# Optimization experiments

Measured on AMD Instinct MI355X. Metric: run time of the kernel, lower is better.

## Reference

```python
import jax, jax.numpy as jnp
import numpy as np

EPS_CR = 0.5      # eps in coding rate
ETA = 0.5
LAMBDA_LAP = 0.3
LN_EPS = 1e-5


def setup_inputs() -> dict:
    key = jax.random.key(0)
    ks = jax.random.split(key, 8)
    n, in_dim, out_dim, d_sub, K1 = 8192, 256, 128, 64, 3
    H = jax.random.normal(ks[0], (n, in_dim), jnp.float32)
    hop_feats = jax.random.normal(ks[1], (K1, n, in_dim), jnp.float32)
    L = jax.random.normal(ks[2], (n, n), jnp.float32) * 0.01
    W_stack = jax.random.normal(ks[3], (K1, d_sub, in_dim), jnp.float32) * 0.05
    W_out = jax.random.normal(ks[4], (out_dim, in_dim), jnp.float32) * 0.05
    threshold = jnp.full((out_dim,), 0.05, jnp.float32)
    ln_gamma = jnp.ones((out_dim,), jnp.float32)
    ln_beta = jnp.zeros((out_dim,), jnp.float32)
    tau = jnp.asarray(1.0, jnp.float32)
    return {"H": H, "hop_feats": hop_feats, "L": L, "W_stack": W_stack,
            "W_out": W_out, "threshold": threshold, "ln_gamma": ln_gamma,
            "ln_beta": ln_beta, "tau": tau}


def reference(H, hop_feats, L, W_stack, W_out, threshold, ln_gamma, ln_beta, tau):
    n = H.shape[0]
    d = W_stack.shape[1]
    coeff = d / (n * EPS_CR * EPS_CR)
    # per-hop subspace projections: Z [K+1, n, d]
    Z = jnp.einsum('knf,kdf->knd', hop_feats, W_stack)
    # shared Gram M = I + coeff * Z^T Z  [K+1, d, d]
    G = jnp.einsum('knd,kne->kde', Z, Z)
    M = jnp.eye(d, dtype=Z.dtype)[None] + coeff * G
    # coding rates via batched slogdet
    _, logdet = jnp.linalg.slogdet(M)
    R = 0.5 * logdet                                    # [K+1]
    # delta_R: first entry is R[0], rest are successive diffs
    delta_R = R - jnp.concatenate([jnp.zeros((1,), R.dtype), R[:-1]])
    dR_norm = (delta_R - delta_R.mean()) / (jnp.std(delta_R, ddof=1) + 1e-6)
    w = jax.nn.softmax(dR_norm / tau)                   # [K+1]
    # coding-rate gradients: g_Z = coeff * Z @ M^{-1} via batched solve
    g_Z = coeff * jnp.linalg.solve(M, jnp.swapaxes(Z, 1, 2))  # [K+1, d, n]
    # g_H[k] = g_Z[k]^T @ W[k]; weighted sum over hops -> [n, in_dim]
    grad_contrib = jnp.einsum('k,kdn,kdf->nf', w, g_Z, W_stack)
    H_half = H + ETA * grad_contrib - ETA * LAMBDA_LAP * (L @ H)
    # in_dim != out_dim -> project
    H_pre = H_half @ W_out.T                            # [n, out_dim]
    thr = jnp.abs(threshold)[None, :]
    H_soft = jnp.sign(H_pre) * jnp.maximum(jnp.abs(H_pre) - thr, 0.0)
    # LayerNorm over last dim
    mu = H_soft.mean(-1, keepdims=True)
    var = jnp.mean((H_soft - mu) ** 2, -1, keepdims=True)
    H_out = (H_soft - mu) * jax.lax.rsqrt(var + LN_EPS) * ln_gamma + ln_beta
    return (H_out, w, jax.lax.stop_gradient(dR_norm), jax.lax.stop_gradient(delta_R))
```

## Files before the change

kernel.cpp:

```cpp
#include <hip/hip_runtime.h>
#include <hip/hip_bf16.h>
#include <math.h>


#define COEFF 0.03125f
#define SCL_LAP (-0.15f)

typedef __attribute__((ext_vector_type(8))) short short8;
typedef __attribute__((ext_vector_type(4))) float f32x4;

__device__ __forceinline__ unsigned short f2bf_bits(float f) {
  unsigned int u = __float_as_uint(f);
  unsigned int r = (u + 0x7fffu + ((u >> 16) & 1u)) >> 16;
  return (unsigned short)r;
}

__global__ __launch_bounds__(256) void gemm_tile(
    const float* __restrict__ A, const float* __restrict__ B,
    float* __restrict__ C, const float* __restrict__ addC,
    const float* __restrict__ scale_ptr,
    int K, int lda, int ldb, int ldc, int ldadd,
    long sA, long sB, long sC, int transB) {
  __shared__ __align__(16) float As[16][68];
  __shared__ __align__(16) float Bs[16][68];
  const int tid = threadIdx.x;
  const int tx = tid & 15, ty = tid >> 4;
  const int m0 = blockIdx.y * 64, n0 = blockIdx.x * 64;
  const int b = blockIdx.z;
  A += (size_t)b * sA; B += (size_t)b * sB; C += (size_t)b * sC;
  float cc[4][4];
#pragma unroll
  for (int i = 0; i < 4; ++i)
#pragma unroll
    for (int j = 0; j < 4; ++j) cc[i][j] = 0.f;
  const int lr = tid >> 2, lc = (tid & 3) << 2;
  for (int k0 = 0; k0 < K; k0 += 16) {
    float4 av = *(const float4*)(A + (size_t)(m0 + lr) * lda + k0 + lc);
    As[lc][lr] = av.x; As[lc + 1][lr] = av.y; As[lc + 2][lr] = av.z; As[lc + 3][lr] = av.w;
    if (transB) {
      float4 bv = *(const float4*)(B + (size_t)(n0 + lr) * ldb + k0 + lc);
      Bs[lc][lr] = bv.x; Bs[lc + 1][lr] = bv.y; Bs[lc + 2][lr] = bv.z; Bs[lc + 3][lr] = bv.w;
    } else {
      int kk = tid & 15, n4 = (tid >> 4) << 2;
      float4 bv = *(const float4*)(B + (size_t)(k0 + kk) * ldb + n0 + n4);
      *(float4*)&Bs[kk][n4] = bv;
    }
    __syncthreads();
#pragma unroll
    for (int kk = 0; kk < 16; ++kk) {
      float4 a4 = *(const float4*)&As[kk][ty * 4];
      float4 b4 = *(const float4*)&Bs[kk][tx * 4];
      float a[4] = {a4.x, a4.y, a4.z, a4.w};
      float bb[4] = {b4.x, b4.y, b4.z, b4.w};
#pragma unroll
      for (int i = 0; i < 4; ++i)
#pragma unroll
        for (int j = 0; j < 4; ++j) cc[i][j] = fmaf(a[i], bb[j], cc[i][j]);
    }
    __syncthreads();
  }
  float scale = scale_ptr ? scale_ptr[b] : 1.0f;
#pragma unroll
  for (int i = 0; i < 4; ++i)
#pragma unroll
    for (int j = 0; j < 4; ++j) {
      int m = m0 + ty * 4 + i, n = n0 + tx * 4 + j;
      float v = cc[i][j] * scale;
      if (addC) v += addC[(size_t)m * ldadd + n];
      C[(size_t)m * ldc + n] = v;
    }
}

__global__ __launch_bounds__(256) void gram_kernel(const float* __restrict__ Z,
                                                   float* __restrict__ Gpart) {
  __shared__ __align__(16) float Zs[64][68];
  const int k = blockIdx.y, tid = threadIdx.x;
  const int d0 = (tid & 15) * 4, e0 = (tid >> 4) * 4;
  float acc[4][4];
#pragma unroll
  for (int i = 0; i < 4; ++i)
#pragma unroll
    for (int j = 0; j < 4; ++j) acc[i][j] = 0.f;
  for (int c = 0; c < 4; ++c) {
    int nb = blockIdx.x * 256 + c * 64;
    for (int idx = tid; idx < 1024; idx += 256) {
      int rr = idx >> 4, c4 = (idx & 15) * 4;
      float4 v = *(const float4*)(Z + (size_t)(nb + rr) * 192 + k * 64 + c4);
      *(float4*)&Zs[rr][c4] = v;
    }
    __syncthreads();
    for (int rr = 0; rr < 64; ++rr) {
      float4 zd4 = *(const float4*)&Zs[rr][d0];
      float4 ze4 = *(const float4*)&Zs[rr][e0];
      float zd[4] = {zd4.x, zd4.y, zd4.z, zd4.w};
      float ze[4] = {ze4.x, ze4.y, ze4.z, ze4.w};
#pragma unroll
      for (int i = 0; i < 4; ++i)
#pragma unroll
        for (int j = 0; j < 4; ++j) acc[i][j] = fmaf(zd[i], ze[j], acc[i][j]);
    }
    __syncthreads();
  }
  float* g = Gpart + (size_t)(k * 32 + blockIdx.x) * 4096;
#pragma unroll
  for (int i = 0; i < 4; ++i)
#pragma unroll
    for (int j = 0; j < 4; ++j) g[(d0 + i) * 64 + (e0 + j)] = acc[i][j];
}

__device__ __forceinline__ float blocksum256(float v, volatile float* scr) {
#pragma unroll
  for (int o = 32; o; o >>= 1) v += __shfl_xor(v, o);
  __syncthreads();
  if ((threadIdx.x & 63) == 0) scr[threadIdx.x >> 6] = v;
  __syncthreads();
  return scr[0] + scr[1] + scr[2] + scr[3];
}

__device__ __forceinline__ void gemm64s(const float* X, const float* Y,
                                        float acc[4][4]) {
  const int tx = threadIdx.x & 15, ty = threadIdx.x >> 4;
#pragma unroll
  for (int i = 0; i < 4; ++i)
#pragma unroll
    for (int j = 0; j < 4; ++j) acc[i][j] = 0.f;
  for (int kk = 0; kk < 64; ++kk) {
    float4 a4 = *(const float4*)&X[kk * 64 + ty * 4];
    float4 b4 = *(const float4*)&Y[kk * 64 + tx * 4];
    float a[4] = {a4.x, a4.y, a4.z, a4.w};
    float bb[4] = {b4.x, b4.y, b4.z, b4.w};
#pragma unroll
    for (int i = 0; i < 4; ++i)
#pragma unroll
      for (int j = 0; j < 4; ++j) acc[i][j] = fmaf(a[i], bb[j], acc[i][j]);
  }
}

__device__ __forceinline__ void wb64(float* D, const float acc[4][4]) {
  const int tx = threadIdx.x & 15, ty = threadIdx.x >> 4;
#pragma unroll
  for (int i = 0; i < 4; ++i)
#pragma unroll
    for (int j = 0; j < 4; ++j) D[(ty * 4 + i) * 64 + tx * 4 + j] = acc[i][j];
}

__device__ __forceinline__ float dot64(const float* X, const float* Y, float* scr) {
  const int tx = threadIdx.x & 15, ty = threadIdx.x >> 4;
  float v = 0.f;
#pragma unroll
  for (int i = 0; i < 4; ++i)
#pragma unroll
    for (int j = 0; j < 4; ++j) {
      int idx = (ty * 4 + i) * 64 + tx * 4 + j;
      v += X[idx] * Y[idx];
    }
  return blocksum256(v, scr);
}

__global__ __launch_bounds__(256) void fused_big(
    const float* __restrict__ Lp, const unsigned short* __restrict__ HpT,
    float* __restrict__ Pbuf, const float* __restrict__ Gpart,
    float* __restrict__ Minv, float* __restrict__ Rout) {
  __shared__ __align__(16) float smem[12304];
  const int tid = threadIdx.x;

  if (blockIdx.x >= 3) {
    unsigned short (*As)[40] = (unsigned short(*)[40])smem;
    unsigned short (*Bs)[40] = (unsigned short(*)[40])(smem + 2560);
    const int g = blockIdx.x - 3;
    const int m0 = (g & 63) * 128;
    const int split = g >> 6;
    const int kbase = split * 1024;
    const int wave = tid >> 6, lane = tid & 63;
    const int ar = tid >> 1, ah = (tid & 1) * 16;
    const size_t lrow = (size_t)(m0 + ar) * 8192;
    const size_t brow = (size_t)ar * 8192;
    f32x4 acc[2][8];
#pragma unroll
    for (int i = 0; i < 2; ++i)
#pragma unroll
      for (int j = 0; j < 8; ++j) acc[i][j] = (f32x4){0.f, 0.f, 0.f, 0.f};
    float4 apf[4];
    uint4 bpf[2];
    {
      const float* ap = Lp + lrow + kbase + ah;
      apf[0] = *(const float4*)(ap); apf[1] = *(const float4*)(ap + 4);
      apf[2] = *(const float4*)(ap + 8); apf[3] = *(const float4*)(ap + 12);
      const unsigned short* bp = HpT + brow + kbase + ah;
      bpf[0] = *(const uint4*)(bp); bpf[1] = *(const uint4*)(bp + 8);
    }
    const int quad = lane >> 4, mcol = lane & 15;
    for (int step = 0; step < 32; ++step) {
      __syncthreads();
      {
        __attribute__((aligned(16))) unsigned short tmp[16];
        const float* f = (const float*)apf;
#pragma unroll
        for (int i = 0; i < 16; ++i) tmp[i] = f2bf_bits(f[i]);
        *(uint4*)&As[ar][ah] = *(const uint4*)&tmp[0];
        *(uint4*)&As[ar][ah + 8] = *(const uint4*)&tmp[8];
        *(uint4*)&Bs[ar][ah] = bpf[0];
        *(uint4*)&Bs[ar][ah + 8] = bpf[1];
      }
      __syncthreads();
      if (step < 31) {
        int kc = kbase + (step + 1) * 32;
        const float* ap = Lp + lrow + kc + ah;
        apf[0] = *(const float4*)(ap); apf[1] = *(const float4*)(ap + 4);
        apf[2] = *(const float4*)(ap + 8); apf[3] = *(const float4*)(ap + 12);
        const unsigned short* bp = HpT + brow + kc + ah;
        bpf[0] = *(const uint4*)(bp); bpf[1] = *(const uint4*)(bp + 8);
      }
      short8 af0 = *(const short8*)&As[wave * 32 + mcol][quad * 8];
      short8 af1 = *(const short8*)&As[wave * 32 + 16 + mcol][quad * 8];
#pragma unroll
      for (int nt = 0; nt < 8; ++nt) {
        short8 bf = *(const short8*)&Bs[nt * 16 + mcol][quad * 8];
        acc[0][nt] = __builtin_amdgcn_mfma_f32_16x16x32_bf16(af0, bf, acc[0][nt], 0, 0, 0);
        acc[1][nt] = __builtin_amdgcn_mfma_f32_16x16x32_bf16(af1, bf, acc[1][nt], 0, 0, 0);
      }
    }
    float* P = Pbuf + (size_t)split * 1048576;
#pragma unroll
    for (int mt = 0; mt < 2; ++mt)
#pragma unroll
      for (int nt = 0; nt < 8; ++nt)
#pragma unroll
        for (int r = 0; r < 4; ++r) {
          int grow = m0 + wave * 32 + mt * 16 + quad * 4 + r;
          int gcol = nt * 16 + mcol;
          P[(size_t)grow * 128 + gcol] = acc[mt][nt][r];
        }
    return;
  }

  const int k = blockIdx.x;
  float* B0 = smem;
  float* B1 = smem + 4096;
  float* B2 = smem + 8192;
  float* scr = smem + 12288;
  for (int i = tid; i < 4096; i += 256) {
    float s = 0.f;
    const float* gp = Gpart + (size_t)k * 32 * 4096 + i;
    for (int b = 0; b < 32; ++b) s += gp[b * 4096];
    B0[i] = COEFF * s + ((i >> 6) == (i & 63) ? 1.f : 0.f);
  }
  __syncthreads();
  if (tid < 64) {
    float rs = 0.f, dg = B0[tid * 65];
    for (int j = 0; j < 64; ++j) rs += fabsf(B0[j * 64 + tid]);
    float lo = 2.f * dg - rs, hi = rs;
#pragma unroll
    for (int o = 32; o; o >>= 1) {
      lo = fminf(lo, __shfl_xor(lo, o));
      hi = fmaxf(hi, __shfl_xor(hi, o));
    }
    if (tid == 0) scr[4] = 0.5f * (fmaxf(lo, 1.f) + hi);
  }
  __syncthreads();
  const float alpha = scr[4], inva = 1.f / alpha;
  for (int i = tid; i < 4096; i += 256) {
    int r = i >> 6, c = i & 63;
    B0[i] = B0[i] * inva - (r == c ? 1.f : 0.f);
  }
  __syncthreads();
  const int tx = tid & 15, ty = tid >> 4;
  float v1 = 0.f, v2 = 0.f;
#pragma unroll
  for (int i = 0; i < 4; ++i)
#pragma unroll
    for (int j = 0; j < 4; ++j) {
      int r = ty * 4 + i, c = tx * 4 + j;
      float e = B0[r * 64 + c];
      if (r == c) v1 += e;
      v2 += e * e;
    }
  float t1 = blocksum256(v1, scr);
  float t2 = blocksum256(v2, scr);
  float acc[4][4];
  gemm64s(B0, B0, acc); __syncthreads(); wb64(B1, acc); __syncthreads();
  float t3 = dot64(B1, B0, scr);
  float t4 = dot64(B1, B1, scr);
  gemm64s(B1, B0, acc); __syncthreads(); wb64(B2, acc); __syncthreads();
  float t5 = dot64(B2, B1, scr);
  float t6 = dot64(B2, B2, scr);
  gemm64s(B1, B1, acc);
  {
    float v7 = 0.f, v8 = 0.f;
#pragma unroll
    for (int i = 0; i < 4; ++i)
#pragma unroll
      for (int j = 0; j < 4; ++j) {
        int idx = (ty * 4 + i) * 64 + tx * 4 + j;
        v7 += acc[i][j] * B2[idx];
        v8 += acc[i][j] * acc[i][j];
      }
    float t7 = blocksum256(v7, scr);
    float t8 = blocksum256(v8, scr);
    if (tid == 0) {
      float ld = 64.f * logf(alpha) + t1 - t2 * 0.5f + t3 / 3.f - t4 * 0.25f
                 + t5 * 0.2f - t6 / 6.f + t7 / 7.f - t8 * 0.125f;
      Rout[k] = 0.5f * ld;
    }
  }
  for (int i = tid; i < 4096; i += 256) {
    int r = i >> 6, c = i & 63;
    B1[i] = (r == c ? 1.f : 0.f) - B0[i];
  }
  __syncthreads();
  for (int it = 0; it < 2; ++it) {
    gemm64s(B0, B1, acc);
    __syncthreads();
    {
#pragma unroll
      for (int i = 0; i < 4; ++i)
#pragma unroll
        for (int j = 0; j < 4; ++j) {
          int idx = (ty * 4 + i) * 64 + tx * 4 + j;
          B2[idx] = acc[i][j] + B1[idx];
        }
    }
    __syncthreads();
    gemm64s(B1, B2, acc);
    __syncthreads();
    {
#pragma unroll
      for (int i = 0; i < 4; ++i)
#pragma unroll
        for (int j = 0; j < 4; ++j) {
          int idx = (ty * 4 + i) * 64 + tx * 4 + j;
          B1[idx] = 2.f * B1[idx] - acc[i][j];
        }
    }
    __syncthreads();
  }
  for (int i = tid; i < 4096; i += 256) Minv[k * 4096 + i] = B1[i] * inva;
}

__global__ void small_w(const float* __restrict__ R, const float* __restrict__ tauP,
                        float* __restrict__ tail, float* __restrict__ sb) {
  if (threadIdx.x != 0) return;
  float R0 = R[0], R1 = R[1], R2 = R[2];
  float d0 = R0, d1 = R1 - R0, d2 = R2 - R1;
  float mean = (d0 + d1 + d2) * (1.f / 3.f);
  float e0 = d0 - mean, e1 = d1 - mean, e2 = d2 - mean;
  float sd = sqrtf((e0 * e0 + e1 * e1 + e2 * e2) * 0.5f) + 1e-6f;
  float n0 = e0 / sd, n1 = e1 / sd, n2 = e2 / sd;
  float tau = tauP[0];
  float x0 = n0 / tau, x1 = n1 / tau, x2 = n2 / tau;
  float mx = fmaxf(x0, fmaxf(x1, x2));
  float w0 = expf(x0 - mx), w1 = expf(x1 - mx), w2 = expf(x2 - mx);
  float s = w0 + w1 + w2;
  w0 /= s; w1 /= s; w2 /= s;
  tail[0] = w0; tail[1] = w1; tail[2] = w2;
  tail[3] = n0; tail[4] = n1; tail[5] = n2;
  tail[6] = d0; tail[7] = d1; tail[8] = d2;
  sb[0] = 0.015625f * w0; sb[1] = 0.015625f * w1; sb[2] = 0.015625f * w2;
}

__global__ __launch_bounds__(256) void transpose_cvt(const float* __restrict__ Hp,
                                                     unsigned short* __restrict__ HpT) {
  __shared__ float T[32][33];
  const int cb = blockIdx.x, rb = blockIdx.y, tid = threadIdx.x;
  int r = tid >> 3, c4 = (tid & 7) * 4;
  float4 v = *(const float4*)(Hp + (size_t)(rb * 32 + r) * 128 + cb * 32 + c4);
  T[r][c4] = v.x; T[r][c4 + 1] = v.y; T[r][c4 + 2] = v.z; T[r][c4 + 3] = v.w;
  __syncthreads();
  int c = tid >> 3, r4 = (tid & 7) * 4;
  ushort4 u;
  u.x = f2bf_bits(T[r4][c]); u.y = f2bf_bits(T[r4 + 1][c]);
  u.z = f2bf_bits(T[r4 + 2][c]); u.w = f2bf_bits(T[r4 + 3][c]);
  *(ushort4*)(HpT + (size_t)(cb * 32 + c) * 8192 + rb * 32 + r4) = u;
}

__global__ __launch_bounds__(256) void finish_kernel(
    const float* __restrict__ pre, const float* __restrict__ Pbuf,
    const float* __restrict__ thr, const float* __restrict__ gamma,
    const float* __restrict__ beta, float* __restrict__ out) {
  const int lane = threadIdx.x & 63;
  const int row = blockIdx.x * 4 + (threadIdx.x >> 6);
  const size_t off = (size_t)row * 128;
  float l0 = 0.f, l1 = 0.f;
#pragma unroll
  for (int s = 0; s < 8; ++s) {
    l0 += Pbuf[s * 1048576 + off + lane];
    l1 += Pbuf[s * 1048576 + off + lane + 64];
  }
  float x0 = pre[off + lane] + SCL_LAP * l0;
  float x1 = pre[off + lane + 64] + SCL_LAP * l1;
  float t0 = fabsf(thr[lane]), t1 = fabsf(thr[lane + 64]);
  float a0 = fmaxf(fabsf(x0) - t0, 0.f); float s0 = (x0 >= 0.f) ? a0 : -a0;
  float a1 = fmaxf(fabsf(x1) - t1, 0.f); float s1 = (x1 >= 0.f) ? a1 : -a1;
  float sum = s0 + s1;
#pragma unroll
  for (int o = 32; o; o >>= 1) sum += __shfl_xor(sum, o);
  float mean = sum * (1.f / 128.f);
  float d0 = s0 - mean, d1 = s1 - mean;
  float ss = d0 * d0 + d1 * d1;
#pragma unroll
  for (int o = 32; o; o >>= 1) ss += __shfl_xor(ss, o);
  float inv = rsqrtf(ss * (1.f / 128.f) + 1e-5f);
  out[off + lane] = d0 * inv * gamma[lane] + beta[lane];
  out[off + lane + 64] = d1 * inv * gamma[lane + 64] + beta[lane + 64];
}

extern "C" void kernel_launch(void* const* d_in, const int* in_sizes, int n_in,
                              void* d_out, int out_size, void* d_ws, size_t ws_size,
                              hipStream_t stream) {
  const float* H = (const float*)d_in[0];
  const float* hop = (const float*)d_in[1];
  const float* L = (const float*)d_in[2];
  const float* Wst = (const float*)d_in[3];
  const float* Wout = (const float*)d_in[4];
  const float* thr = (const float*)d_in[5];
  const float* gamma = (const float*)d_in[6];
  const float* beta = (const float*)d_in[7];
  const float* tau = (const float*)d_in[8];
  float* out = (float*)d_out;

  float* ws = (float*)d_ws;
  float* Zbuf = ws;
  float* Hp = Zbuf + 1572864;
  float* pre = Hp + 1048576;
  float* Gpart = pre + 1048576;
  float* Minv = Gpart + 393216;
  float* Rb = Minv + 12288;
  float* sb = Rb + 16;
  float* Pb = sb + 16;
  float* QT = Pb + 24576;
  float* Pbuf = QT + 24576;
  unsigned short* HpT = (unsigned short*)(Pbuf + 8388608);

  gemm_tile<<<dim3(2, 128, 1), 256, 0, stream>>>(
      H, Wout, Hp, nullptr, nullptr, 256, 256, 256, 128, 0, 0L, 0L, 0L, 1);
  transpose_cvt<<<dim3(4, 256), 256, 0, stream>>>(Hp, HpT);
  gemm_tile<<<dim3(1, 128, 3), 256, 0, stream>>>(
      hop, Wst, Zbuf, nullptr, nullptr, 256, 256, 256, 192, 0,
      2097152L, 16384L, 64L, 1);
  gram_kernel<<<dim3(32, 3), 256, 0, stream>>>(Zbuf, Gpart);
  gemm_tile<<<dim3(1, 2, 3), 256, 0, stream>>>(
      Wout, Wst, Pb, nullptr, nullptr, 256, 256, 256, 64, 0,
      0L, 16384L, 8192L, 1);
  fused_big<<<dim3(515), 256, 0, stream>>>(L, HpT, Pbuf, Gpart, Minv, Rb);
  small_w<<<dim3(1), 64, 0, stream>>>(Rb, tau, out + 1048576, sb);
  gemm_tile<<<dim3(1, 2, 3), 256, 0, stream>>>(
      Pb, Minv, QT, nullptr, sb, 64, 64, 64, 192, 0,
      8192L, 4096L, 64L, 0);
  gemm_tile<<<dim3(2, 128, 1), 256, 0, stream>>>(
      Zbuf, QT, pre, Hp, nullptr, 192, 192, 192, 128, 128, 0L, 0L, 0L, 1);
  finish_kernel<<<dim3(2048), 256, 0, stream>>>(pre, Pbuf, thr, gamma, beta, out);

  (void)in_sizes; (void)n_in; (void)out_size; (void)ws_size;
}
```

Measured before the change: 559.8 us.

## Fuse projection/transpose, Z/Gram, final GEMM/LayerNorm and double-buffer L GEMM

Fuses the H@Wout projection with the bf16 transpose, the per-hop Z projection with the Gram partial sums, and the final Z@QT GEMM with the Laplacian reduction, soft-threshold and LayerNorm. The fused_big bf16 MFMA loop now uses two LDS buffers with a two-step prefetch, so there is one barrier per step instead of two. Together these drop three launches and the round trips of Hp, Z and the pre buffer through global memory. In exchange the Gram partials grow to 128 per hop, making the reduction in fused_big longer, and the L GEMM needs more LDS and registers.

```diff
diff --git a/kernel.cpp b/kernel.cpp
--- a/kernel.cpp
+++ b/kernel.cpp
@@ -17,9 +17,8 @@
 
 __global__ __launch_bounds__(256) void gemm_tile(
     const float* __restrict__ A, const float* __restrict__ B,
-    float* __restrict__ C, const float* __restrict__ addC,
-    const float* __restrict__ scale_ptr,
-    int K, int lda, int ldb, int ldc, int ldadd,
+    float* __restrict__ C, const float* __restrict__ scale_ptr,
+    int K, int lda, int ldb, int ldc,
     long sA, long sB, long sC, int transB) {
   __shared__ __align__(16) float As[16][68];
   __shared__ __align__(16) float Bs[16][68];
@@ -63,49 +62,120 @@
 #pragma unroll
   for (int i = 0; i < 4; ++i)
 #pragma unroll
-    for (int j = 0; j < 4; ++j) {
-      int m = m0 + ty * 4 + i, n = n0 + tx * 4 + j;
-      float v = cc[i][j] * scale;
-      if (addC) v += addC[(size_t)m * ldadd + n];
-      C[(size_t)m * ldc + n] = v;
-    }
-}
-
-__global__ __launch_bounds__(256) void gram_kernel(const float* __restrict__ Z,
-                                                   float* __restrict__ Gpart) {
-  __shared__ __align__(16) float Zs[64][68];
-  const int k = blockIdx.y, tid = threadIdx.x;
+    for (int j = 0; j < 4; ++j)
+      C[(size_t)(m0 + ty * 4 + i) * ldc + n0 + tx * 4 + j] = cc[i][j] * scale;
+}
+
+__global__ __launch_bounds__(256) void hp_kernel(
+    const float* __restrict__ H, const float* __restrict__ Wout,
+    float* __restrict__ Hp, unsigned short* __restrict__ HpT) {
+  __shared__ __align__(16) float As[16][68];
+  __shared__ __align__(16) float Bs[16][68];
+  const int tid = threadIdx.x;
+  const int tx = tid & 15, ty = tid >> 4;
+  const int m0 = blockIdx.y * 64, n0 = blockIdx.x * 64;
+  float cc[4][4];
+#pragma unroll
+  for (int i = 0; i < 4; ++i)
+#pragma unroll
+    for (int j = 0; j < 4; ++j) cc[i][j] = 0.f;
+  const int lr = tid >> 2, lc = (tid & 3) << 2;
+  for (int k0 = 0; k0 < 256; k0 += 16) {
+    float4 av = *(const float4*)(H + (size_t)(m0 + lr) * 256 + k0 + lc);
+    As[lc][lr] = av.x; As[lc + 1][lr] = av.y; As[lc + 2][lr] = av.z; As[lc + 3][lr] = av.w;
+    float4 bv = *(const float4*)(Wout + (size_t)(n0 + lr) * 256 + k0 + lc);
+    Bs[lc][lr] = bv.x; Bs[lc + 1][lr] = bv.y; Bs[lc + 2][lr] = bv.z; Bs[lc + 3][lr] = bv.w;
+    __syncthreads();
+#pragma unroll
+    for (int kk = 0; kk < 16; ++kk) {
+      float4 a4 = *(const float4*)&As[kk][ty * 4];
+      float4 b4 = *(const float4*)&Bs[kk][tx * 4];
+      float a[4] = {a4.x, a4.y, a4.z, a4.w};
+      float bb[4] = {b4.x, b4.y, b4.z, b4.w};
+#pragma unroll
+      for (int i = 0; i < 4; ++i)
+#pragma unroll
+        for (int j = 0; j < 4; ++j) cc[i][j] = fmaf(a[i], bb[j], cc[i][j]);
+    }
+    __syncthreads();
+  }
+#pragma unroll
+  for (int i = 0; i < 4; ++i)
+    *(float4*)(Hp + (size_t)(m0 + ty * 4 + i) * 128 + n0 + tx * 4) =
+        (float4){cc[i][0], cc[i][1], cc[i][2], cc[i][3]};
+#pragma unroll
+  for (int j = 0; j < 4; ++j) {
+    ushort4 u;
+    u.x = f2bf_bits(cc[0][j]); u.y = f2bf_bits(cc[1][j]);
+    u.z = f2bf_bits(cc[2][j]); u.w = f2bf_bits(cc[3][j]);
+    *(ushort4*)(HpT + (size_t)(n0 + tx * 4 + j) * 8192 + m0 + ty * 4) = u;
+  }
+}
+
+__global__ __launch_bounds__(256) void zgram(
+    const float* __restrict__ hop, const float* __restrict__ Wst,
+    float* __restrict__ Zbuf, float* __restrict__ Gpart) {
+  __shared__ __align__(16) float sm[4352];
+  float (*As)[68] = (float(*)[68])sm;
+  float (*Bs)[68] = (float(*)[68])(sm + 1088);
+  float (*Zs)[68] = (float(*)[68])sm;
+  const int tid = threadIdx.x;
+  const int tx = tid & 15, ty = tid >> 4;
+  const int m0 = blockIdx.x * 64, k = blockIdx.y;
+  const float* A = hop + (size_t)k * 2097152;
+  const float* B = Wst + (size_t)k * 16384;
+  float cc[4][4];
+#pragma unroll
+  for (int i = 0; i < 4; ++i)
+#pragma unroll
+    for (int j = 0; j < 4; ++j) cc[i][j] = 0.f;
+  const int lr = tid >> 2, lc = (tid & 3) << 2;
+  for (int k0 = 0; k0 < 256; k0 += 16) {
+    float4 av = *(const float4*)(A + (size_t)(m0 + lr) * 256 + k0 + lc);
+    As[lc][lr] = av.x; As[lc + 1][lr] = av.y; As[lc + 2][lr] = av.z; As[lc + 3][lr] = av.w;
+    float4 bv = *(const float4*)(B + (size_t)lr * 256 + k0 + lc);
+    Bs[lc][lr] = bv.x; Bs[lc + 1][lr] = bv.y; Bs[lc + 2][lr] = bv.z; Bs[lc + 3][lr] = bv.w;
+    __syncthreads();
+#pragma unroll
+    for (int kk = 0; kk < 16; ++kk) {
+      float4 a4 = *(const float4*)&As[kk][ty * 4];
+      float4 b4 = *(const float4*)&Bs[kk][tx * 4];
+      float a[4] = {a4.x, a4.y, a4.z, a4.w};
+      float bb[4] = {b4.x, b4.y, b4.z, b4.w};
+#pragma unroll
+      for (int i = 0; i < 4; ++i)
+#pragma unroll
+        for (int j = 0; j < 4; ++j) cc[i][j] = fmaf(a[i], bb[j], cc[i][j]);
+    }
+    __syncthreads();
+  }
+#pragma unroll
+  for (int i = 0; i < 4; ++i) {
+    float4 v = {cc[i][0], cc[i][1], cc[i][2], cc[i][3]};
+    *(float4*)(Zbuf + (size_t)(m0 + ty * 4 + i) * 192 + k * 64 + tx * 4) = v;
+    *(float4*)&Zs[ty * 4 + i][tx * 4] = v;
+  }
+  __syncthreads();
   const int d0 = (tid & 15) * 4, e0 = (tid >> 4) * 4;
   float acc[4][4];
 #pragma unroll
   for (int i = 0; i < 4; ++i)
 #pragma unroll
     for (int j = 0; j < 4; ++j) acc[i][j] = 0.f;
-  for (int c = 0; c < 4; ++c) {
-    int nb = blockIdx.x * 256 + c * 64;
-    for (int idx = tid; idx < 1024; idx += 256) {
-      int rr = idx >> 4, c4 = (idx & 15) * 4;
-      float4 v = *(const float4*)(Z + (size_t)(nb + rr) * 192 + k * 64 + c4);
-      *(float4*)&Zs[rr][c4] = v;
-    }
-    __syncthreads();
-    for (int rr = 0; rr < 64; ++rr) {
-      float4 zd4 = *(const float4*)&Zs[rr][d0];
-      float4 ze4 = *(const float4*)&Zs[rr][e0];
-      float zd[4] = {zd4.x, zd4.y, zd4.z, zd4.w};
-      float ze[4] = {ze4.x, ze4.y, ze4.z, ze4.w};
-#pragma unroll
-      for (int i = 0; i < 4; ++i)
-#pragma unroll
-        for (int j = 0; j < 4; ++j) acc[i][j] = fmaf(zd[i], ze[j], acc[i][j]);
-    }
-    __syncthreads();
-  }
-  float* g = Gpart + (size_t)(k * 32 + blockIdx.x) * 4096;
-#pragma unroll
-  for (int i = 0; i < 4; ++i)
-#pragma unroll
-    for (int j = 0; j < 4; ++j) g[(d0 + i) * 64 + (e0 + j)] = acc[i][j];
+  for (int rr = 0; rr < 64; ++rr) {
+    float4 zd4 = *(const float4*)&Zs[rr][d0];
+    float4 ze4 = *(const float4*)&Zs[rr][e0];
+    float zd[4] = {zd4.x, zd4.y, zd4.z, zd4.w};
+    float ze[4] = {ze4.x, ze4.y, ze4.z, ze4.w};
+#pragma unroll
+    for (int i = 0; i < 4; ++i)
+#pragma unroll
+      for (int j = 0; j < 4; ++j) acc[i][j] = fmaf(zd[i], ze[j], acc[i][j]);
+  }
+  float* g = Gpart + (size_t)(k * 128 + blockIdx.x) * 4096;
+#pragma unroll
+  for (int i = 0; i < 4; ++i)
+    *(float4*)(g + (d0 + i) * 64 + e0) = (float4){acc[i][0], acc[i][1], acc[i][2], acc[i][3]};
 }
 
 __device__ __forceinline__ float blocksum256(float v, volatile float* scr) {
@@ -165,12 +235,10 @@
   const int tid = threadIdx.x;
 
   if (blockIdx.x >= 3) {
-    unsigned short (*As)[40] = (unsigned short(*)[40])smem;
-    unsigned short (*Bs)[40] = (unsigned short(*)[40])(smem + 2560);
+    unsigned short* sm = (unsigned short*)smem;
     const int g = blockIdx.x - 3;
     const int m0 = (g & 63) * 128;
-    const int split = g >> 6;
-    const int kbase = split * 1024;
+    const int kbase = (g >> 6) * 1024;
     const int wave = tid >> 6, lane = tid & 63;
     const int ar = tid >> 1, ah = (tid & 1) * 16;
     const size_t lrow = (size_t)(m0 + ar) * 8192;
@@ -180,37 +248,40 @@
     for (int i = 0; i < 2; ++i)
 #pragma unroll
       for (int j = 0; j < 8; ++j) acc[i][j] = (f32x4){0.f, 0.f, 0.f, 0.f};
-    float4 apf[4];
-    uint4 bpf[2];
-    {
-      const float* ap = Lp + lrow + kbase + ah;
-      apf[0] = *(const float4*)(ap); apf[1] = *(const float4*)(ap + 4);
-      apf[2] = *(const float4*)(ap + 8); apf[3] = *(const float4*)(ap + 12);
-      const unsigned short* bp = HpT + brow + kbase + ah;
-      bpf[0] = *(const uint4*)(bp); bpf[1] = *(const uint4*)(bp + 8);
+    float4 apf[2][4];
+    uint4 bpf[2][2];
+#pragma unroll
+    for (int p = 0; p < 2; ++p) {
+      const float* ap = Lp + lrow + kbase + p * 32 + ah;
+      apf[p][0] = *(const float4*)(ap); apf[p][1] = *(const float4*)(ap + 4);
+      apf[p][2] = *(const float4*)(ap + 8); apf[p][3] = *(const float4*)(ap + 12);
+      const unsigned short* bp = HpT + brow + kbase + p * 32 + ah;
+      bpf[p][0] = *(const uint4*)(bp); bpf[p][1] = *(const uint4*)(bp + 8);
     }
     const int quad = lane >> 4, mcol = lane & 15;
     for (int step = 0; step < 32; ++step) {
-      __syncthreads();
+      const int b = step & 1;
+      unsigned short (*As)[40] = (unsigned short(*)[40])(sm + b * 5120);
+      unsigned short (*Bs)[40] = (unsigned short(*)[40])(sm + 10240 + b * 5120);
       {
         __attribute__((aligned(16))) unsigned short tmp[16];
-        const float* f = (const float*)apf;
+        const float* f = (const float*)apf[b];
 #pragma unroll
         for (int i = 0; i < 16; ++i) tmp[i] = f2bf_bits(f[i]);
         *(uint4*)&As[ar][ah] = *(const uint4*)&tmp[0];
         *(uint4*)&As[ar][ah + 8] = *(const uint4*)&tmp[8];
-        *(uint4*)&Bs[ar][ah] = bpf[0];
-        *(uint4*)&Bs[ar][ah + 8] = bpf[1];
+        *(uint4*)&Bs[ar][ah] = bpf[b][0];
+        *(uint4*)&Bs[ar][ah + 8] = bpf[b][1];
+      }
+      if (step < 30) {
+        int kc = kbase + (step + 2) * 32;
+        const float* ap = Lp + lrow + kc + ah;
+        apf[b][0] = *(const float4*)(ap); apf[b][1] = *(const float4*)(ap + 4);
+        apf[b][2] = *(const float4*)(ap + 8); apf[b][3] = *(const float4*)(ap + 12);
+        const unsigned short* bp = HpT + brow + kc + ah;
+        bpf[b][0] = *(const uint4*)(bp); bpf[b][1] = *(const uint4*)(bp + 8);
       }
       __syncthreads();
-      if (step < 31) {
-        int kc = kbase + (step + 1) * 32;
-        const float* ap = Lp + lrow + kc + ah;
-        apf[0] = *(const float4*)(ap); apf[1] = *(const float4*)(ap + 4);
-        apf[2] = *(const float4*)(ap + 8); apf[3] = *(const float4*)(ap + 12);
-        const unsigned short* bp = HpT + brow + kc + ah;
-        bpf[0] = *(const uint4*)(bp); bpf[1] = *(const uint4*)(bp + 8);
-      }
       short8 af0 = *(const short8*)&As[wave * 32 + mcol][quad * 8];
       short8 af1 = *(const short8*)&As[wave * 32 + 16 + mcol][quad * 8];
 #pragma unroll
@@ -220,7 +291,7 @@
         acc[1][nt] = __builtin_amdgcn_mfma_f32_16x16x32_bf16(af1, bf, acc[1][nt], 0, 0, 0);
       }
     }
-    float* P = Pbuf + (size_t)split * 1048576;
+    float* P = Pbuf + (size_t)(g >> 6) * 1048576;
 #pragma unroll
     for (int mt = 0; mt < 2; ++mt)
 #pragma unroll
@@ -239,11 +310,23 @@
   float* B1 = smem + 4096;
   float* B2 = smem + 8192;
   float* scr = smem + 12288;
-  for (int i = tid; i < 4096; i += 256) {
-    float s = 0.f;
-    const float* gp = Gpart + (size_t)k * 32 * 4096 + i;
-    for (int b = 0; b < 32; ++b) s += gp[b * 4096];
-    B0[i] = COEFF * s + ((i >> 6) == (i & 63) ? 1.f : 0.f);
+  {
+    const float* gp = Gpart + (size_t)k * 524288 + tid * 16;
+    float4 s0 = {0,0,0,0}, s1 = {0,0,0,0}, s2 = {0,0,0,0}, s3 = {0,0,0,0};
+    for (int b = 0; b < 128; ++b) {
+      const float4* p = (const float4*)(gp + (size_t)b * 4096);
+      s0.x += p[0].x; s0.y += p[0].y; s0.z += p[0].z; s0.w += p[0].w;
+      s1.x += p[1].x; s1.y += p[1].y; s1.z += p[1].z; s1.w += p[1].w;
+      s2.x += p[2].x; s2.y += p[2].y; s2.z += p[2].z; s2.w += p[2].w;
+      s3.x += p[3].x; s3.y += p[3].y; s3.z += p[3].z; s3.w += p[3].w;
+    }
+    float vals[16] = {s0.x, s0.y, s0.z, s0.w, s1.x, s1.y, s1.z, s1.w,
+                      s2.x, s2.y, s2.z, s2.w, s3.x, s3.y, s3.z, s3.w};
+#pragma unroll
+    for (int t = 0; t < 16; ++t) {
+      int i = tid * 16 + t;
+      B0[i] = COEFF * vals[t] + ((i >> 6) == (i & 63) ? 1.f : 0.f);
+    }
   }
   __syncthreads();
   if (tid < 64) {
@@ -311,27 +394,23 @@
   for (int it = 0; it < 2; ++it) {
     gemm64s(B0, B1, acc);
     __syncthreads();
-    {
-#pragma unroll
-      for (int i = 0; i < 4; ++i)
-#pragma unroll
-        for (int j = 0; j < 4; ++j) {
-          int idx = (ty * 4 + i) * 64 + tx * 4 + j;
-          B2[idx] = acc[i][j] + B1[idx];
-        }
-    }
+#pragma unroll
+    for (int i = 0; i < 4; ++i)
+#pragma unroll
+      for (int j = 0; j < 4; ++j) {
+        int idx = (ty * 4 + i) * 64 + tx * 4 + j;
+        B2[idx] = acc[i][j] + B1[idx];
+      }
     __syncthreads();
     gemm64s(B1, B2, acc);
     __syncthreads();
-    {
-#pragma unroll
-      for (int i = 0; i < 4; ++i)
-#pragma unroll
-        for (int j = 0; j < 4; ++j) {
-          int idx = (ty * 4 + i) * 64 + tx * 4 + j;
-          B1[idx] = 2.f * B1[idx] - acc[i][j];
-        }
-    }
+#pragma unroll
+    for (int i = 0; i < 4; ++i)
+#pragma unroll
+      for (int j = 0; j < 4; ++j) {
+        int idx = (ty * 4 + i) * 64 + tx * 4 + j;
+        B1[idx] = 2.f * B1[idx] - acc[i][j];
+      }
     __syncthreads();
   }
   for (int i = tid; i < 4096; i += 256) Minv[k * 4096 + i] = B1[i] * inva;
@@ -358,50 +437,109 @@
   sb[0] = 0.015625f * w0; sb[1] = 0.015625f * w1; sb[2] = 0.015625f * w2;
 }
 
-__global__ __launch_bounds__(256) void transpose_cvt(const float* __restrict__ Hp,
-                                                     unsigned short* __restrict__ HpT) {
-  __shared__ float T[32][33];
-  const int cb = blockIdx.x, rb = blockIdx.y, tid = threadIdx.x;
-  int r = tid >> 3, c4 = (tid & 7) * 4;
-  float4 v = *(const float4*)(Hp + (size_t)(rb * 32 + r) * 128 + cb * 32 + c4);
-  T[r][c4] = v.x; T[r][c4 + 1] = v.y; T[r][c4 + 2] = v.z; T[r][c4 + 3] = v.w;
-  __syncthreads();
-  int c = tid >> 3, r4 = (tid & 7) * 4;
-  ushort4 u;
-  u.x = f2bf_bits(T[r4][c]); u.y = f2bf_bits(T[r4 + 1][c]);
-  u.z = f2bf_bits(T[r4 + 2][c]); u.w = f2bf_bits(T[r4 + 3][c]);
-  *(ushort4*)(HpT + (size_t)(cb * 32 + c) * 8192 + rb * 32 + r4) = u;
-}
-
-__global__ __launch_bounds__(256) void finish_kernel(
-    const float* __restrict__ pre, const float* __restrict__ Pbuf,
+__global__ __launch_bounds__(256) void pre_finish(
+    const float* __restrict__ Zb, const float* __restrict__ QT,
+    const float* __restrict__ Hp, const float* __restrict__ Pbuf,
     const float* __restrict__ thr, const float* __restrict__ gamma,
     const float* __restrict__ beta, float* __restrict__ out) {
-  const int lane = threadIdx.x & 63;
-  const int row = blockIdx.x * 4 + (threadIdx.x >> 6);
-  const size_t off = (size_t)row * 128;
-  float l0 = 0.f, l1 = 0.f;
-#pragma unroll
-  for (int s = 0; s < 8; ++s) {
-    l0 += Pbuf[s * 1048576 + off + lane];
-    l1 += Pbuf[s * 1048576 + off + lane + 64];
-  }
-  float x0 = pre[off + lane] + SCL_LAP * l0;
-  float x1 = pre[off + lane + 64] + SCL_LAP * l1;
-  float t0 = fabsf(thr[lane]), t1 = fabsf(thr[lane + 64]);
-  float a0 = fmaxf(fabsf(x0) - t0, 0.f); float s0 = (x0 >= 0.f) ? a0 : -a0;
-  float a1 = fmaxf(fabsf(x1) - t1, 0.f); float s1 = (x1 >= 0.f) ? a1 : -a1;
-  float sum = s0 + s1;
-#pragma unroll
-  for (int o = 32; o; o >>= 1) sum += __shfl_xor(sum, o);
-  float mean = sum * (1.f / 128.f);
-  float d0 = s0 - mean, d1 = s1 - mean;
-  float ss = d0 * d0 + d1 * d1;
-#pragma unroll
-  for (int o = 32; o; o >>= 1) ss += __shfl_xor(ss, o);
-  float inv = rsqrtf(ss * (1.f / 128.f) + 1e-5f);
-  out[off + lane] = d0 * inv * gamma[lane] + beta[lane];
-  out[off + lane + 64] = d1 * inv * gamma[lane + 64] + beta[lane + 64];
+  __shared__ __align__(16) float As[16][36];
+  __shared__ __align__(16) float Bs[16][132];
+  const int tid = threadIdx.x;
+  const int tx = tid & 31, ty = tid >> 5;
+  const int m0 = blockIdx.x * 32;
+  float cc[4][4];
+#pragma unroll
+  for (int i = 0; i < 4; ++i)
+#pragma unroll
+    for (int j = 0; j < 4; ++j) cc[i][j] = 0.f;
+  for (int k0 = 0; k0 < 192; k0 += 16) {
+    if (tid < 128) {
+      int row = tid >> 2, c4 = (tid & 3) * 4;
+      float4 v = *(const float4*)(Zb + (size_t)(m0 + row) * 192 + k0 + c4);
+      As[c4][row] = v.x; As[c4 + 1][row] = v.y; As[c4 + 2][row] = v.z; As[c4 + 3][row] = v.w;
+    }
+#pragma unroll
+    for (int t = 0; t < 2; ++t) {
+      int idx = tid + t * 256;
+      int n = idx >> 2, c4 = (idx & 3) * 4;
+      float4 v = *(const float4*)(QT + (size_t)n * 192 + k0 + c4);
+      Bs[c4][n] = v.x; Bs[c4 + 1][n] = v.y; Bs[c4 + 2][n] = v.z; Bs[c4 + 3][n] = v.w;
+    }
+    __syncthreads();
+#pragma unroll
+    for (int kk = 0; kk < 16; ++kk) {
+      float4 a4 = *(const float4*)&As[kk][ty * 4];
+      float4 b4 = *(const float4*)&Bs[kk][tx * 4];
+      float a[4] = {a4.x, a4.y, a4.z, a4.w};
+      float bb[4] = {b4.x, b4.y, b4.z, b4.w};
+#pragma unroll
+      for (int i = 0; i < 4; ++i)
+#pragma unroll
+        for (int j = 0; j < 4; ++j) cc[i][j] = fmaf(a[i], bb[j], cc[i][j]);
+    }
+    __syncthreads();
+  }
+  float4 tv = *(const float4*)(thr + tx * 4);
+  float tj[4] = {fabsf(tv.x), fabsf(tv.y), fabsf(tv.z), fabsf(tv.w)};
+  float sth[4][4], rs[4];
+#pragma unroll
+  for (int i = 0; i < 4; ++i) {
+    const size_t off = (size_t)(m0 + ty * 4 + i) * 128 + tx * 4;
+    float4 h = *(const float4*)(Hp + off);
+    float x[4] = {h.x, h.y, h.z, h.w};
+    float4 l0 = {0, 0, 0, 0};
+#pragma unroll
+    for (int s = 0; s < 8; ++s) {
+      float4 p = *(const float4*)(Pbuf + (size_t)s * 1048576 + off);
+      l0.x += p.x; l0.y += p.y; l0.z += p.z; l0.w += p.w;
+    }
+    x[0] += cc[i][0] + SCL_LAP * l0.x;
+    x[1] += cc[i][1] + SCL_LAP * l0.y;
+    x[2] += cc[i][2] + SCL_LAP * l0.z;
+    x[3] += cc[i][3] + SCL_LAP * l0.w;
+    float lsum = 0.f;
+#pragma unroll
+    for (int j = 0; j < 4; ++j) {
+      float a = fmaxf(fabsf(x[j]) - tj[j], 0.f);
+      sth[i][j] = (x[j] >= 0.f) ? a : -a;
+      lsum += sth[i][j];
+    }
+    rs[i] = lsum;
+  }
+#pragma unroll
+  for (int o = 16; o; o >>= 1)
+#pragma unroll
+    for (int i = 0; i < 4; ++i) rs[i] += __shfl_xor(rs[i], o);
+  float var[4];
+#pragma unroll
+  for (int i = 0; i < 4; ++i) {
+    float mean = rs[i] * (1.f / 128.f);
+    float v = 0.f;
+#pragma unroll
+    for (int j = 0; j < 4; ++j) {
+      sth[i][j] -= mean;
+      v += sth[i][j] * sth[i][j];
+    }
+    var[i] = v;
+  }
+#pragma unroll
+  for (int o = 16; o; o >>= 1)
+#pragma unroll
+    for (int i = 0; i < 4; ++i) var[i] += __shfl_xor(var[i], o);
+  float4 gv = *(const float4*)(gamma + tx * 4);
+  float4 bv = *(const float4*)(beta + tx * 4);
+  float gj[4] = {gv.x, gv.y, gv.z, gv.w};
+  float bj[4] = {bv.x, bv.y, bv.z, bv.w};
+#pragma unroll
+  for (int i = 0; i < 4; ++i) {
+    float inv = rsqrtf(var[i] * (1.f / 128.f) + 1e-5f);
+    float4 o4;
+    o4.x = sth[i][0] * inv * gj[0] + bj[0];
+    o4.y = sth[i][1] * inv * gj[1] + bj[1];
+    o4.z = sth[i][2] * inv * gj[2] + bj[2];
+    o4.w = sth[i][3] * inv * gj[3] + bj[3];
+    *(float4*)(out + (size_t)(m0 + ty * 4 + i) * 128 + tx * 4) = o4;
+  }
 }
 
 extern "C" void kernel_launch(void* const* d_in, const int* in_sizes, int n_in,
@@ -421,9 +559,8 @@
   float* ws = (float*)d_ws;
   float* Zbuf = ws;
   float* Hp = Zbuf + 1572864;
-  float* pre = Hp + 1048576;
-  float* Gpart = pre + 1048576;
-  float* Minv = Gpart + 393216;
+  float* Gpart = Hp + 1048576;
+  float* Minv = Gpart + 1572864;
   float* Rb = Minv + 12288;
   float* sb = Rb + 16;
   float* Pb = sb + 16;
@@ -431,24 +568,15 @@
   float* Pbuf = QT + 24576;
   unsigned short* HpT = (unsigned short*)(Pbuf + 8388608);
 
-  gemm_tile<<<dim3(2, 128, 1), 256, 0, stream>>>(
-      H, Wout, Hp, nullptr, nullptr, 256, 256, 256, 128, 0, 0L, 0L, 0L, 1);
-  transpose_cvt<<<dim3(4, 256), 256, 0, stream>>>(Hp, HpT);
-  gemm_tile<<<dim3(1, 128, 3), 256, 0, stream>>>(
-      hop, Wst, Zbuf, nullptr, nullptr, 256, 256, 256, 192, 0,
-      2097152L, 16384L, 64L, 1);
-  gram_kernel<<<dim3(32, 3), 256, 0, stream>>>(Zbuf, Gpart);
+  hp_kernel<<<dim3(2, 128), 256, 0, stream>>>(H, Wout, Hp, HpT);
+  zgram<<<dim3(128, 3), 256, 0, stream>>>(hop, Wst, Zbuf, Gpart);
   gemm_tile<<<dim3(1, 2, 3), 256, 0, stream>>>(
-      Wout, Wst, Pb, nullptr, nullptr, 256, 256, 256, 64, 0,
-      0L, 16384L, 8192L, 1);
+      Wout, Wst, Pb, nullptr, 256, 256, 256, 64, 0L, 16384L, 8192L, 1);
   fused_big<<<dim3(515), 256, 0, stream>>>(L, HpT, Pbuf, Gpart, Minv, Rb);
   small_w<<<dim3(1), 64, 0, stream>>>(Rb, tau, out + 1048576, sb);
   gemm_tile<<<dim3(1, 2, 3), 256, 0, stream>>>(
-      Pb, Minv, QT, nullptr, sb, 64, 64, 64, 192, 0,
-      8192L, 4096L, 64L, 0);
-  gemm_tile<<<dim3(2, 128, 1), 256, 0, stream>>>(
-      Zbuf, QT, pre, Hp, nullptr, 192, 192, 192, 128, 128, 0L, 0L, 0L, 1);
-  finish_kernel<<<dim3(2048), 256, 0, stream>>>(pre, Pbuf, thr, gamma, beta, out);
+      Pb, Minv, QT, sb, 64, 64, 64, 192, 8192L, 4096L, 64L, 0);
+  pre_finish<<<dim3(256), 256, 0, stream>>>(Zbuf, QT, Hp, Pbuf, thr, gamma, beta, out);
 
   (void)in_sizes; (void)n_in; (void)out_size; (void)ws_size;
 }
```

Measured after the change: 650.3 us. 16.2% more time.
